# Kernel tuning notes

Measured on AMD Instinct MI355X. Metric: run time of the kernel, lower is better.

## Reference

```python
import jax, jax.numpy as jnp
import numpy as np

D, H, W, C = 24, 24, 16, 2        # image_dims + num_classes
THETA_ALPHA = 160.0               # bilateral spatial std
THETA_BETA = 3.0                  # bilateral intensity std
THETA_GAMMA = 3.0                 # spatial-only std
NUM_ITERATIONS = 5
N = D * H * W


def _gauss_kernel(feats):
    # Dense Gaussian kernel K_ij = exp(-0.5 * ||f_i - f_j||^2).
    # This is the exact filter that the permutohedral lattice approximates
    # (self-term included, matching the lattice splat/blur/slice behaviour).
    sq = jnp.sum(feats * feats, axis=-1)               # [N]
    d2 = sq[:, None] + sq[None, :] - 2.0 * feats @ feats.T
    return jnp.exp(-0.5 * jnp.maximum(d2, 0.0))        # [N, N]


def _positions():
    zz, yy, xx = jnp.meshgrid(jnp.arange(D), jnp.arange(H), jnp.arange(W), indexing='ij')
    return jnp.stack([zz, yy, xx], axis=-1).reshape(N, 3).astype(jnp.float32)


def setup_inputs() -> dict:
    key = jax.random.key(0)
    k1, k2 = jax.random.split(key)
    unaries = jax.random.normal(k1, (1, D, H, W, C), dtype=jnp.float32)
    rgb = jax.random.uniform(k2, (1, D, H, W, 1), dtype=jnp.float32)
    # learned params (build() initial values)
    spatial_ker_weights = jnp.array([1.41, 1.41], dtype=jnp.float32)
    bilateral_ker_weights = jnp.array([3.85, 3.85], dtype=jnp.float32)
    compatibility_matrix = jnp.eye(C, dtype=jnp.float32)
    return dict(unaries=unaries, rgb=rgb,
                spatial_ker_weights=spatial_ker_weights,
                bilateral_ker_weights=bilateral_ker_weights,
                compatibility_matrix=compatibility_matrix)


def reference(unaries, rgb, spatial_ker_weights, bilateral_ker_weights, compatibility_matrix):
    out_shape = unaries.shape
    u = unaries.reshape(N, C)                 # batch index 0 only, as in the TF code
    img = rgb.reshape(N, -1)
    pos = _positions()

    Ks = _gauss_kernel(pos / THETA_GAMMA)                                        # spatial kernel [N,N]
    Kb = _gauss_kernel(jnp.concatenate([pos / THETA_ALPHA, img / THETA_BETA], -1))  # bilateral kernel [N,N]

    # normalization = filter applied to all-ones (row sums)
    norm_s = jnp.sum(Ks, axis=-1, keepdims=True)   # [N,1]
    norm_b = jnp.sum(Kb, axis=-1, keepdims=True)   # [N,1]

    q = u
    for _ in range(NUM_ITERATIONS):
        spatial_out = (Ks @ q) / norm_s            # [N,C]
        bilateral_out = (Kb @ q) / norm_b          # [N,C]
        # diag(w_s) @ spatial.T + diag(w_b) @ bilateral.T  ==  per-class scaling
        message = spatial_out * spatial_ker_weights + bilateral_out * bilateral_ker_weights
        pairwise = message @ compatibility_matrix.T  # (compat @ msg.T).T
        q = u - pairwise
    return q.reshape(out_shape)
```

## Files before the change

### kernel.cpp

```cpp
#include <hip/hip_runtime.h>


#define DD 24
#define HH 24
#define WW 16
#define SLICE 384
#define NPTS 9216
#define NT 5
#define NF_ITER 12
#define LOG2E 1.4426950408889634f
#define K3L   (LOG2E / 18.0f)
#define K160L (LOG2E / 51200.0f)

static __device__ __forceinline__ int iabs(int a) { return a < 0 ? -a : a; }

__global__ __launch_bounds__(SLICE)
void xy_kernel(const float2* __restrict__ qsrc,
               const float* __restrict__ rgb,
               float* __restrict__ tmp, int mode) {
    __shared__ float g[DD];
    __shared__ float a[SLICE];
    __shared__ float b[SLICE];
    const int z = blockIdx.x;
    const int f = blockIdx.y;
    const int t = threadIdx.x;

    const bool spatial = (mode == 1) && (f < 2);
    const float k2 = spatial ? K3L : K160L;
    if (t < DD) g[t] = exp2f(-(float)(t * t) * k2);

    const int i = z * SLICE + t;
    float v;
    if (mode == 0) {
        float I3 = rgb[i] * (1.0f / 3.0f);
        float E = exp2f(-0.5f * LOG2E * I3 * I3);
        float P = E;
        for (int s = 0; s < f; ++s) P *= I3;
        v = P;
    } else {
        float2 q = qsrc[i];
        if (f < 2) {
            v = (f == 0) ? q.x : q.y;
        } else {
            int tt = (f - 2) >> 1;
            int c  = (f - 2) & 1;
            float I3 = rgb[i] * (1.0f / 3.0f);
            float E = exp2f(-0.5f * LOG2E * I3 * I3);
            float P = E;
            for (int s = 0; s < tt; ++s) P *= I3;
            v = P * (c ? q.y : q.x);
        }
    }
    a[t] = v;
    __syncthreads();

    const int y = t >> 4, x = t & 15;
    float s = 0.f;
#pragma unroll
    for (int xp = 0; xp < WW; ++xp)
        s = fmaf(g[iabs(x - xp)], a[(y << 4) + xp], s);
    b[t] = s;
    __syncthreads();

    float s2 = 0.f;
#pragma unroll
    for (int yp = 0; yp < HH; ++yp)
        s2 = fmaf(g[iabs(y - yp)], b[(yp << 4) + x], s2);
    tmp[f * NPTS + i] = s2;
}

__global__ __launch_bounds__(256)
void z_norm_kernel(const float* __restrict__ tmp,
                   const float* __restrict__ rgb,
                   float* __restrict__ norm_b) {
    __shared__ float gz[DD];
    const int tid = threadIdx.x;
    const int i = blockIdx.x * 256 + tid;
    const int z = i / SLICE;
    const int yx = i - z * SLICE;
    if (tid < DD) gz[tid] = exp2f(-(float)(tid * tid) * K160L);
    __syncthreads();

    float acc[NT] = {0.f, 0.f, 0.f, 0.f, 0.f};
    for (int zp = 0; zp < DD; ++zp) {
        float w = gz[iabs(z - zp)];
        const float* base = tmp + zp * SLICE + yx;
#pragma unroll
        for (int t = 0; t < NT; ++t) acc[t] = fmaf(w, base[t * NPTS], acc[t]);
    }
    const float invf[NT] = {1.f, 1.f, 0.5f, 1.f / 6.f, 1.f / 24.f};
    float I3 = rgb[i] * (1.0f / 3.0f);
    float P = exp2f(-0.5f * LOG2E * I3 * I3);
    float nb = 0.f;
#pragma unroll
    for (int t = 0; t < NT; ++t) { nb = fmaf(P * invf[t], acc[t], nb); P *= I3; }
    norm_b[i] = nb;
}

__global__ __launch_bounds__(256)
void z_iter_kernel(const float* __restrict__ tmp,
                   const float* __restrict__ rgb,
                   const float* __restrict__ norm_b,
                   const float2* __restrict__ u2,
                   const float* __restrict__ sw,
                   const float* __restrict__ bw,
                   const float* __restrict__ compat,
                   float2* __restrict__ qdst,
                   float2* __restrict__ out) {
    __shared__ float g3[DD];
    __shared__ float g160[DD];
    __shared__ float ssx[WW];
    __shared__ float ssy[HH];
    const int tid = threadIdx.x;
    const int i = blockIdx.x * 256 + tid;
    const int z = i / SLICE;
    const int yx = i - z * SLICE;
    const int y = yx >> 4, x = yx & 15;

    if (tid < DD) g3[tid] = exp2f(-(float)(tid * tid) * K3L);
    else if (tid >= 32 && tid < 32 + DD) {
        int d = tid - 32;
        g160[d] = exp2f(-(float)(d * d) * K160L);
    }
    __syncthreads();
    if (tid < WW) {
        float s = 0.f;
        for (int xp = 0; xp < WW; ++xp) s += g3[iabs(tid - xp)];
        ssx[tid] = s;
    } else if (tid >= 64 && tid < 64 + HH) {
        int yy = tid - 64;
        float s = 0.f;
        for (int yp = 0; yp < HH; ++yp) s += g3[iabs(yy - yp)];
        ssy[yy] = s;
    }
    __syncthreads();

    float acc[NF_ITER];
#pragma unroll
    for (int f = 0; f < NF_ITER; ++f) acc[f] = 0.f;
    for (int zp = 0; zp < DD; ++zp) {
        float w3 = g3[iabs(z - zp)];
        float wb = g160[iabs(z - zp)];
        const float* base = tmp + zp * SLICE + yx;
        acc[0] = fmaf(w3, base[0 * NPTS], acc[0]);
        acc[1] = fmaf(w3, base[1 * NPTS], acc[1]);
#pragma unroll
        for (int f = 2; f < NF_ITER; ++f) acc[f] = fmaf(wb, base[f * NPTS], acc[f]);
    }

    float inv_ns = 1.0f / (ssy[z] * ssy[y] * ssx[x]);
    float s0 = acc[0] * inv_ns;
    float s1 = acc[1] * inv_ns;

    const float invf[NT] = {1.f, 1.f, 0.5f, 1.f / 6.f, 1.f / 24.f};
    float I3 = rgb[i] * (1.0f / 3.0f);
    float P = exp2f(-0.5f * LOG2E * I3 * I3);
    float b0 = 0.f, b1 = 0.f;
#pragma unroll
    for (int t = 0; t < NT; ++t) {
        float w = P * invf[t];
        b0 = fmaf(w, acc[2 + 2 * t], b0);
        b1 = fmaf(w, acc[3 + 2 * t], b1);
        P *= I3;
    }
    float inv_nb = 1.0f / norm_b[i];
    b0 *= inv_nb;
    b1 *= inv_nb;

    float m0 = s0 * sw[0] + b0 * bw[0];
    float m1 = s1 * sw[1] + b1 * bw[1];
    float p0 = fmaf(compat[0], m0, compat[1] * m1);
    float p1 = fmaf(compat[2], m0, compat[3] * m1);
    float2 uu = u2[i];
    float2 qn = make_float2(uu.x - p0, uu.y - p1);
    qdst[i] = qn;
    if (out != nullptr) out[i] = qn;
}

extern "C" void kernel_launch(void* const* d_in, const int* in_sizes, int n_in,
                              void* d_out, int out_size, void* d_ws, size_t ws_size,
                              hipStream_t stream) {
    const float*  u      = (const float*)d_in[0];
    const float*  rgb    = (const float*)d_in[1];
    const float*  sw     = (const float*)d_in[2];
    const float*  bw     = (const float*)d_in[3];
    const float*  compat = (const float*)d_in[4];
    const float2* u2     = (const float2*)u;
    float2* out = (float2*)d_out;

    float* ws = (float*)d_ws;
    float*  tmp    = ws;
    float*  norm_b = ws + NF_ITER * NPTS;
    float2* qbuf   = (float2*)(ws + (NF_ITER + 1) * NPTS);

    xy_kernel<<<dim3(DD, NT), SLICE, 0, stream>>>(nullptr, rgb, tmp, 0);
    z_norm_kernel<<<NPTS / 256, 256, 0, stream>>>(tmp, rgb, norm_b);

    for (int it = 0; it < 5; ++it) {
        const float2* qsrc = (it == 0) ? u2 : (const float2*)qbuf;
        xy_kernel<<<dim3(DD, NF_ITER), SLICE, 0, stream>>>(qsrc, rgb, tmp, 1);
        z_iter_kernel<<<NPTS / 256, 256, 0, stream>>>(tmp, rgb, norm_b, u2,
                                                      sw, bw, compat, qbuf,
                                                      (it == 4) ? out : nullptr);
    }
}
```

Measured before the change: 118.1 us.

## Fuse all CRF stages into one persistent kernel with grid barriers

Replaces the twelve separate launches (xy, z_norm, and five xy/z_iter pairs) with one persistent 24-block kernel that keeps per-point state in registers and synchronises between stages with an atomic grid barrier. The intermediate layout changes to point-major with 12 interleaved features read and written as float4, and all 12 features are convolved in one block per z-slice rather than one block per feature. The aim is to remove launch and inter-kernel gaps. In exchange only 24 workgroups run, using a small fraction of the GPU, and the kernel relies on all blocks being co-resident for the spin barrier.

```diff
diff --git a/kernel.cpp b/kernel.cpp
--- a/kernel.cpp
+++ b/kernel.cpp
@@ -7,200 +7,259 @@
 #define SLICE 384
 #define NPTS 9216
 #define NT 5
-#define NF_ITER 12
+#define TP 12
+#define NP 8
+#define LPITCH 196
+#define NBLOCKS 24
 #define LOG2E 1.4426950408889634f
 #define K3L   (LOG2E / 18.0f)
 #define K160L (LOG2E / 51200.0f)
 
 static __device__ __forceinline__ int iabs(int a) { return a < 0 ? -a : a; }
 
-__global__ __launch_bounds__(SLICE)
-void xy_kernel(const float2* __restrict__ qsrc,
-               const float* __restrict__ rgb,
-               float* __restrict__ tmp, int mode) {
-    __shared__ float g[DD];
-    __shared__ float a[SLICE];
-    __shared__ float b[SLICE];
+__global__ void init_bar_kernel(unsigned* bar) {
+    if (threadIdx.x < 8) bar[threadIdx.x] = 0u;
+}
+
+static __device__ __forceinline__ void gridbar(unsigned* bar, int phase) {
+    __syncthreads();
+    if (threadIdx.x == 0) {
+        __threadfence();
+        __hip_atomic_fetch_add(&bar[phase], 1u, __ATOMIC_ACQ_REL,
+                               __HIP_MEMORY_SCOPE_AGENT);
+        while (__hip_atomic_load(&bar[phase], __ATOMIC_ACQUIRE,
+                                 __HIP_MEMORY_SCOPE_AGENT) < (unsigned)NBLOCKS) {
+            __builtin_amdgcn_s_sleep(1);
+        }
+        __threadfence();
+    }
+    __syncthreads();
+}
+
+static __device__ __forceinline__ void xy_conv12(
+        float* sA, float* sB, const float* g3, const float* g160,
+        int y, int x, const float v[12], float ov[12]) {
+    float4* wrow = (float4*)(sA + y * LPITCH + x * 12);
+    wrow[0] = make_float4(v[0], v[1], v[2], v[3]);
+    wrow[1] = make_float4(v[4], v[5], v[6], v[7]);
+    wrow[2] = make_float4(v[8], v[9], v[10], v[11]);
+    __syncthreads();
+
+    float ax[12];
+#pragma unroll
+    for (int f = 0; f < 12; ++f) ax[f] = 0.f;
+    const float4* rowy = (const float4*)(sA + y * LPITCH);
+#pragma unroll
+    for (int xp = 0; xp < WW; ++xp) {
+        int d = iabs(x - xp);
+        float w3 = g3[d], wb = g160[d];
+        float4 a0 = rowy[xp * 3 + 0];
+        float4 a1 = rowy[xp * 3 + 1];
+        float4 a2 = rowy[xp * 3 + 2];
+        ax[0] = fmaf(w3, a0.x, ax[0]);  ax[1] = fmaf(w3, a0.y, ax[1]);
+        ax[2] = fmaf(wb, a0.z, ax[2]);  ax[3] = fmaf(wb, a0.w, ax[3]);
+        ax[4] = fmaf(wb, a1.x, ax[4]);  ax[5] = fmaf(wb, a1.y, ax[5]);
+        ax[6] = fmaf(wb, a1.z, ax[6]);  ax[7] = fmaf(wb, a1.w, ax[7]);
+        ax[8] = fmaf(wb, a2.x, ax[8]);  ax[9] = fmaf(wb, a2.y, ax[9]);
+        ax[10] = fmaf(wb, a2.z, ax[10]); ax[11] = fmaf(wb, a2.w, ax[11]);
+    }
+    float4* wrowB = (float4*)(sB + y * LPITCH + x * 12);
+    wrowB[0] = make_float4(ax[0], ax[1], ax[2], ax[3]);
+    wrowB[1] = make_float4(ax[4], ax[5], ax[6], ax[7]);
+    wrowB[2] = make_float4(ax[8], ax[9], ax[10], ax[11]);
+    __syncthreads();
+
+#pragma unroll
+    for (int f = 0; f < 12; ++f) ov[f] = 0.f;
+#pragma unroll
+    for (int yp = 0; yp < HH; ++yp) {
+        int d = iabs(y - yp);
+        float w3 = g3[d], wb = g160[d];
+        const float4* col = (const float4*)(sB + yp * LPITCH + x * 12);
+        float4 b0 = col[0];
+        float4 b1 = col[1];
+        float4 b2 = col[2];
+        ov[0] = fmaf(w3, b0.x, ov[0]);  ov[1] = fmaf(w3, b0.y, ov[1]);
+        ov[2] = fmaf(wb, b0.z, ov[2]);  ov[3] = fmaf(wb, b0.w, ov[3]);
+        ov[4] = fmaf(wb, b1.x, ov[4]);  ov[5] = fmaf(wb, b1.y, ov[5]);
+        ov[6] = fmaf(wb, b1.z, ov[6]);  ov[7] = fmaf(wb, b1.w, ov[7]);
+        ov[8] = fmaf(wb, b2.x, ov[8]);  ov[9] = fmaf(wb, b2.y, ov[9]);
+        ov[10] = fmaf(wb, b2.z, ov[10]); ov[11] = fmaf(wb, b2.w, ov[11]);
+    }
+    __syncthreads();
+}
+
+__global__ __launch_bounds__(384, 1)
+void crf_persist(const float2* __restrict__ u2, const float* __restrict__ rgb,
+                 const float* __restrict__ sw, const float* __restrict__ bw,
+                 const float* __restrict__ compat,
+                 float* __restrict__ tmpA, float* __restrict__ tmpB,
+                 float* __restrict__ tmpN, unsigned* __restrict__ bar,
+                 float2* __restrict__ out) {
+    __shared__ float g3[32];
+    __shared__ float g160[32];
+    __shared__ float sA[HH * LPITCH];
+    __shared__ float sB[HH * LPITCH];
+
     const int z = blockIdx.x;
-    const int f = blockIdx.y;
     const int t = threadIdx.x;
-
-    const bool spatial = (mode == 1) && (f < 2);
-    const float k2 = spatial ? K3L : K160L;
-    if (t < DD) g[t] = exp2f(-(float)(t * t) * k2);
-
+    const int y = t >> 4;
+    const int x = t & 15;
     const int i = z * SLICE + t;
-    float v;
-    if (mode == 0) {
-        float I3 = rgb[i] * (1.0f / 3.0f);
-        float E = exp2f(-0.5f * LOG2E * I3 * I3);
-        float P = E;
-        for (int s = 0; s < f; ++s) P *= I3;
-        v = P;
-    } else {
-        float2 q = qsrc[i];
-        if (f < 2) {
-            v = (f == 0) ? q.x : q.y;
-        } else {
-            int tt = (f - 2) >> 1;
-            int c  = (f - 2) & 1;
-            float I3 = rgb[i] * (1.0f / 3.0f);
-            float E = exp2f(-0.5f * LOG2E * I3 * I3);
-            float P = E;
-            for (int s = 0; s < tt; ++s) P *= I3;
-            v = P * (c ? q.y : q.x);
-        }
-    }
-    a[t] = v;
-    __syncthreads();
-
-    const int y = t >> 4, x = t & 15;
-    float s = 0.f;
-#pragma unroll
-    for (int xp = 0; xp < WW; ++xp)
-        s = fmaf(g[iabs(x - xp)], a[(y << 4) + xp], s);
-    b[t] = s;
-    __syncthreads();
-
-    float s2 = 0.f;
-#pragma unroll
-    for (int yp = 0; yp < HH; ++yp)
-        s2 = fmaf(g[iabs(y - yp)], b[(yp << 4) + x], s2);
-    tmp[f * NPTS + i] = s2;
-}
-
-__global__ __launch_bounds__(256)
-void z_norm_kernel(const float* __restrict__ tmp,
-                   const float* __restrict__ rgb,
-                   float* __restrict__ norm_b) {
-    __shared__ float gz[DD];
-    const int tid = threadIdx.x;
-    const int i = blockIdx.x * 256 + tid;
-    const int z = i / SLICE;
-    const int yx = i - z * SLICE;
-    if (tid < DD) gz[tid] = exp2f(-(float)(tid * tid) * K160L);
-    __syncthreads();
-
-    float acc[NT] = {0.f, 0.f, 0.f, 0.f, 0.f};
-    for (int zp = 0; zp < DD; ++zp) {
-        float w = gz[iabs(z - zp)];
-        const float* base = tmp + zp * SLICE + yx;
-#pragma unroll
-        for (int t = 0; t < NT; ++t) acc[t] = fmaf(w, base[t * NPTS], acc[t]);
-    }
+
+    if (t < DD) {
+        g3[t] = exp2f(-(float)(t * t) * K3L);
+        g160[t] = exp2f(-(float)(t * t) * K160L);
+    }
+    __syncthreads();
+
+    float sx = 0.f, sy = 0.f, sz = 0.f;
+    for (int xp = 0; xp < WW; ++xp) sx += g3[iabs(x - xp)];
+    for (int yp = 0; yp < HH; ++yp) sy += g3[iabs(y - yp)];
+    for (int zp = 0; zp < DD; ++zp) sz += g3[iabs(z - zp)];
+    const float inv_ns = 1.0f / (sx * sy * sz);
+    const float I3 = rgb[i] * (1.0f / 3.0f);
+    const float E = exp2f(-0.5f * LOG2E * I3 * I3);
+    const float2 uu = u2[i];
+    const float sw0 = sw[0], sw1 = sw[1];
+    const float bw0 = bw[0], bw1 = bw[1];
+    const float c00 = compat[0], c01 = compat[1];
+    const float c10 = compat[2], c11 = compat[3];
     const float invf[NT] = {1.f, 1.f, 0.5f, 1.f / 6.f, 1.f / 24.f};
-    float I3 = rgb[i] * (1.0f / 3.0f);
-    float P = exp2f(-0.5f * LOG2E * I3 * I3);
-    float nb = 0.f;
-#pragma unroll
-    for (int t = 0; t < NT; ++t) { nb = fmaf(P * invf[t], acc[t], nb); P *= I3; }
-    norm_b[i] = nb;
-}
-
-__global__ __launch_bounds__(256)
-void z_iter_kernel(const float* __restrict__ tmp,
-                   const float* __restrict__ rgb,
-                   const float* __restrict__ norm_b,
-                   const float2* __restrict__ u2,
-                   const float* __restrict__ sw,
-                   const float* __restrict__ bw,
-                   const float* __restrict__ compat,
-                   float2* __restrict__ qdst,
-                   float2* __restrict__ out) {
-    __shared__ float g3[DD];
-    __shared__ float g160[DD];
-    __shared__ float ssx[WW];
-    __shared__ float ssy[HH];
-    const int tid = threadIdx.x;
-    const int i = blockIdx.x * 256 + tid;
-    const int z = i / SLICE;
-    const int yx = i - z * SLICE;
-    const int y = yx >> 4, x = yx & 15;
-
-    if (tid < DD) g3[tid] = exp2f(-(float)(tid * tid) * K3L);
-    else if (tid >= 32 && tid < 32 + DD) {
-        int d = tid - 32;
-        g160[d] = exp2f(-(float)(d * d) * K160L);
-    }
-    __syncthreads();
-    if (tid < WW) {
-        float s = 0.f;
-        for (int xp = 0; xp < WW; ++xp) s += g3[iabs(tid - xp)];
-        ssx[tid] = s;
-    } else if (tid >= 64 && tid < 64 + HH) {
-        int yy = tid - 64;
-        float s = 0.f;
-        for (int yp = 0; yp < HH; ++yp) s += g3[iabs(yy - yp)];
-        ssy[yy] = s;
-    }
-    __syncthreads();
-
-    float acc[NF_ITER];
-#pragma unroll
-    for (int f = 0; f < NF_ITER; ++f) acc[f] = 0.f;
-    for (int zp = 0; zp < DD; ++zp) {
-        float w3 = g3[iabs(z - zp)];
-        float wb = g160[iabs(z - zp)];
-        const float* base = tmp + zp * SLICE + yx;
-        acc[0] = fmaf(w3, base[0 * NPTS], acc[0]);
-        acc[1] = fmaf(w3, base[1 * NPTS], acc[1]);
-#pragma unroll
-        for (int f = 2; f < NF_ITER; ++f) acc[f] = fmaf(wb, base[f * NPTS], acc[f]);
-    }
-
-    float inv_ns = 1.0f / (ssy[z] * ssy[y] * ssx[x]);
-    float s0 = acc[0] * inv_ns;
-    float s1 = acc[1] * inv_ns;
-
-    const float invf[NT] = {1.f, 1.f, 0.5f, 1.f / 6.f, 1.f / 24.f};
-    float I3 = rgb[i] * (1.0f / 3.0f);
-    float P = exp2f(-0.5f * LOG2E * I3 * I3);
-    float b0 = 0.f, b1 = 0.f;
-#pragma unroll
-    for (int t = 0; t < NT; ++t) {
-        float w = P * invf[t];
-        b0 = fmaf(w, acc[2 + 2 * t], b0);
-        b1 = fmaf(w, acc[3 + 2 * t], b1);
-        P *= I3;
-    }
-    float inv_nb = 1.0f / norm_b[i];
-    b0 *= inv_nb;
-    b1 *= inv_nb;
-
-    float m0 = s0 * sw[0] + b0 * bw[0];
-    float m1 = s1 * sw[1] + b1 * bw[1];
-    float p0 = fmaf(compat[0], m0, compat[1] * m1);
-    float p1 = fmaf(compat[2], m0, compat[3] * m1);
-    float2 uu = u2[i];
-    float2 qn = make_float2(uu.x - p0, uu.y - p1);
-    qdst[i] = qn;
-    if (out != nullptr) out[i] = qn;
+    float Pt[NT];
+    Pt[0] = E;
+#pragma unroll
+    for (int k = 1; k < NT; ++k) Pt[k] = Pt[k - 1] * I3;
+
+    float v[12], ov[12];
+
+#pragma unroll
+    for (int f = 0; f < 12; ++f) v[f] = 0.f;
+#pragma unroll
+    for (int k = 0; k < NT; ++k) v[2 + k] = Pt[k];
+    xy_conv12(sA, sB, g3, g160, y, x, v, ov);
+    {
+        float* pn = tmpN + (size_t)i * NP;
+        *(float4*)pn = make_float4(ov[2], ov[3], ov[4], ov[5]);
+        pn[4] = ov[6];
+    }
+    float q0 = uu.x, q1 = uu.y;
+    v[0] = q0; v[1] = q1;
+#pragma unroll
+    for (int k = 0; k < NT; ++k) { v[2 + 2 * k] = Pt[k] * q0; v[3 + 2 * k] = Pt[k] * q1; }
+    xy_conv12(sA, sB, g3, g160, y, x, v, ov);
+    {
+        float4* pd = (float4*)(tmpA + (size_t)i * TP);
+        pd[0] = make_float4(ov[0], ov[1], ov[2], ov[3]);
+        pd[1] = make_float4(ov[4], ov[5], ov[6], ov[7]);
+        pd[2] = make_float4(ov[8], ov[9], ov[10], ov[11]);
+    }
+    gridbar(bar, 0);
+
+    float inv_nb = 0.f;
+    const float* tsrc = tmpA;
+    float* tdst = tmpB;
+
+    for (int it = 0; it < 5; ++it) {
+        if (it == 0) {
+            float accN[NT] = {0.f, 0.f, 0.f, 0.f, 0.f};
+            const float* pn = tmpN + (size_t)t * NP;
+            for (int zp = 0; zp < DD; ++zp) {
+                float wb = g160[iabs(z - zp)];
+                float4 n0 = *(const float4*)pn;
+                float n4 = pn[4];
+                accN[0] = fmaf(wb, n0.x, accN[0]);
+                accN[1] = fmaf(wb, n0.y, accN[1]);
+                accN[2] = fmaf(wb, n0.z, accN[2]);
+                accN[3] = fmaf(wb, n0.w, accN[3]);
+                accN[4] = fmaf(wb, n4, accN[4]);
+                pn += (size_t)SLICE * NP;
+            }
+            float nb = 0.f;
+#pragma unroll
+            for (int k = 0; k < NT; ++k) nb = fmaf(Pt[k] * invf[k], accN[k], nb);
+            inv_nb = 1.0f / nb;
+        }
+
+        float acc[12];
+#pragma unroll
+        for (int f = 0; f < 12; ++f) acc[f] = 0.f;
+        {
+            const float* p = tsrc + (size_t)t * TP;
+            for (int zp = 0; zp < DD; ++zp) {
+                int d = iabs(z - zp);
+                float w3 = g3[d], wb = g160[d];
+                float4 a0 = ((const float4*)p)[0];
+                float4 a1 = ((const float4*)p)[1];
+                float4 a2 = ((const float4*)p)[2];
+                acc[0] = fmaf(w3, a0.x, acc[0]);  acc[1] = fmaf(w3, a0.y, acc[1]);
+                acc[2] = fmaf(wb, a0.z, acc[2]);  acc[3] = fmaf(wb, a0.w, acc[3]);
+                acc[4] = fmaf(wb, a1.x, acc[4]);  acc[5] = fmaf(wb, a1.y, acc[5]);
+                acc[6] = fmaf(wb, a1.z, acc[6]);  acc[7] = fmaf(wb, a1.w, acc[7]);
+                acc[8] = fmaf(wb, a2.x, acc[8]);  acc[9] = fmaf(wb, a2.y, acc[9]);
+                acc[10] = fmaf(wb, a2.z, acc[10]); acc[11] = fmaf(wb, a2.w, acc[11]);
+                p += (size_t)SLICE * TP;
+            }
+        }
+
+        float s0 = acc[0] * inv_ns;
+        float s1 = acc[1] * inv_ns;
+        float b0 = 0.f, b1 = 0.f;
+#pragma unroll
+        for (int k = 0; k < NT; ++k) {
+            float w = Pt[k] * invf[k];
+            b0 = fmaf(w, acc[2 + 2 * k], b0);
+            b1 = fmaf(w, acc[3 + 2 * k], b1);
+        }
+        b0 *= inv_nb;
+        b1 *= inv_nb;
+        float m0 = s0 * sw0 + b0 * bw0;
+        float m1 = s1 * sw1 + b1 * bw1;
+        float p0 = fmaf(c00, m0, c01 * m1);
+        float p1 = fmaf(c10, m0, c11 * m1);
+        q0 = uu.x - p0;
+        q1 = uu.y - p1;
+
+        if (it == 4) {
+            out[i] = make_float2(q0, q1);
+            break;
+        }
+
+        v[0] = q0; v[1] = q1;
+#pragma unroll
+        for (int k = 0; k < NT; ++k) { v[2 + 2 * k] = Pt[k] * q0; v[3 + 2 * k] = Pt[k] * q1; }
+        xy_conv12(sA, sB, g3, g160, y, x, v, ov);
+        {
+            float4* pd = (float4*)(tdst + (size_t)i * TP);
+            pd[0] = make_float4(ov[0], ov[1], ov[2], ov[3]);
+            pd[1] = make_float4(ov[4], ov[5], ov[6], ov[7]);
+            pd[2] = make_float4(ov[8], ov[9], ov[10], ov[11]);
+        }
+        gridbar(bar, 1 + it);
+
+        const float* ns = tdst;
+        tdst = (float*)tsrc;
+        tsrc = ns;
+    }
 }
 
 extern "C" void kernel_launch(void* const* d_in, const int* in_sizes, int n_in,
                               void* d_out, int out_size, void* d_ws, size_t ws_size,
                               hipStream_t stream) {
-    const float*  u      = (const float*)d_in[0];
+    const float2* u2     = (const float2*)d_in[0];
     const float*  rgb    = (const float*)d_in[1];
     const float*  sw     = (const float*)d_in[2];
     const float*  bw     = (const float*)d_in[3];
     const float*  compat = (const float*)d_in[4];
-    const float2* u2     = (const float2*)u;
     float2* out = (float2*)d_out;
 
     float* ws = (float*)d_ws;
-    float*  tmp    = ws;
-    float*  norm_b = ws + NF_ITER * NPTS;
-    float2* qbuf   = (float2*)(ws + (NF_ITER + 1) * NPTS);
-
-    xy_kernel<<<dim3(DD, NT), SLICE, 0, stream>>>(nullptr, rgb, tmp, 0);
-    z_norm_kernel<<<NPTS / 256, 256, 0, stream>>>(tmp, rgb, norm_b);
-
-    for (int it = 0; it < 5; ++it) {
-        const float2* qsrc = (it == 0) ? u2 : (const float2*)qbuf;
-        xy_kernel<<<dim3(DD, NF_ITER), SLICE, 0, stream>>>(qsrc, rgb, tmp, 1);
-        z_iter_kernel<<<NPTS / 256, 256, 0, stream>>>(tmp, rgb, norm_b, u2,
-                                                      sw, bw, compat, qbuf,
-                                                      (it == 4) ? out : nullptr);
-    }
-}
+    float* tmpA = ws;
+    float* tmpB = ws + NPTS * TP;
+    float* tmpN = ws + 2 * NPTS * TP;
+    unsigned* bar = (unsigned*)(ws + 2 * NPTS * TP + NPTS * NP);
+
+    init_bar_kernel<<<1, 64, 0, stream>>>(bar);
+    crf_persist<<<NBLOCKS, 384, 0, stream>>>(u2, rgb, sw, bw, compat,
+                                             tmpA, tmpB, tmpN, bar, out);
+}
```

After: 155.9 us. 1.32x slower.

## Split z-convolution into its own per-feature kernel and merge norm pass into iteration

Applied to the files above, without the earlier changes.

The z-axis Gaussian convolution is moved out of the pointwise update kernel into a separate kernel launched over a grid of slice by feature, so each thread accumulates a single feature instead of twelve. The normalisation features are folded into the first iteration's xy and z passes, which drops the separate norm kernel. Padded shared arrays are used for the xy pass. The cost is one extra launch per iteration and an extra round trip of the intermediate buffer through global memory, in exchange for more parallelism in the z reduction.

```diff
diff --git a/kernel.cpp b/kernel.cpp
--- a/kernel.cpp
+++ b/kernel.cpp
@@ -7,7 +7,8 @@
 #define SLICE 384
 #define NPTS 9216
 #define NT 5
-#define NF_ITER 12
+#define NFI 12
+#define NFT 17
 #define LOG2E 1.4426950408889634f
 #define K3L   (LOG2E / 18.0f)
 #define K160L (LOG2E / 51200.0f)
@@ -15,192 +16,158 @@
 static __device__ __forceinline__ int iabs(int a) { return a < 0 ? -a : a; }
 
 __global__ __launch_bounds__(SLICE)
-void xy_kernel(const float2* __restrict__ qsrc,
-               const float* __restrict__ rgb,
-               float* __restrict__ tmp, int mode) {
-    __shared__ float g[DD];
-    __shared__ float a[SLICE];
-    __shared__ float b[SLICE];
-    const int z = blockIdx.x;
-    const int f = blockIdx.y;
-    const int t = threadIdx.x;
+void k_xy(const float2* __restrict__ qsrc, const float* __restrict__ rgb,
+          float* __restrict__ tmp) {
+    __shared__ float gk[32];
+    __shared__ float sA[HH][WW + 1];
+    __shared__ float sB[HH][WW + 1];
+    const int z = blockIdx.x, f = blockIdx.y, t = threadIdx.x;
+    const int y = t >> 4, x = t & 15;
+    const int i = z * SLICE + t;
 
-    const bool spatial = (mode == 1) && (f < 2);
-    const float k2 = spatial ? K3L : K160L;
-    if (t < DD) g[t] = exp2f(-(float)(t * t) * k2);
+    const float kk = (f < 2) ? K3L : K160L;
+    if (t < DD) gk[t] = exp2f(-(float)(t * t) * kk);
 
-    const int i = z * SLICE + t;
     float v;
-    if (mode == 0) {
-        float I3 = rgb[i] * (1.0f / 3.0f);
+    if (f < 2) {
+        float2 q = qsrc[i];
+        v = (f == 0) ? q.x : q.y;
+    } else {
+        float I3 = rgb[i] * (1.f / 3.f);
         float E = exp2f(-0.5f * LOG2E * I3 * I3);
+        int k = (f < NFI) ? ((f - 2) >> 1) : (f - NFI);
         float P = E;
-        for (int s = 0; s < f; ++s) P *= I3;
-        v = P;
-    } else {
-        float2 q = qsrc[i];
-        if (f < 2) {
-            v = (f == 0) ? q.x : q.y;
+        for (int s = 0; s < k; ++s) P *= I3;
+        if (f < NFI) {
+            float2 q = qsrc[i];
+            v = P * (((f - 2) & 1) ? q.y : q.x);
         } else {
-            int tt = (f - 2) >> 1;
-            int c  = (f - 2) & 1;
-            float I3 = rgb[i] * (1.0f / 3.0f);
-            float E = exp2f(-0.5f * LOG2E * I3 * I3);
-            float P = E;
-            for (int s = 0; s < tt; ++s) P *= I3;
-            v = P * (c ? q.y : q.x);
+            v = P;
         }
     }
-    a[t] = v;
+    sA[y][x] = v;
     __syncthreads();
 
-    const int y = t >> 4, x = t & 15;
-    float s = 0.f;
+    float a = 0.f;
 #pragma unroll
-    for (int xp = 0; xp < WW; ++xp)
-        s = fmaf(g[iabs(x - xp)], a[(y << 4) + xp], s);
-    b[t] = s;
+    for (int xp = 0; xp < WW; ++xp) a = fmaf(gk[iabs(x - xp)], sA[y][xp], a);
+    sB[y][x] = a;
     __syncthreads();
 
-    float s2 = 0.f;
+    float b = 0.f;
 #pragma unroll
-    for (int yp = 0; yp < HH; ++yp)
-        s2 = fmaf(g[iabs(y - yp)], b[(yp << 4) + x], s2);
-    tmp[f * NPTS + i] = s2;
+    for (int yp = 0; yp < HH; ++yp) b = fmaf(gk[iabs(y - yp)], sB[yp][x], b);
+    tmp[f * NPTS + i] = b;
+}
+
+__global__ __launch_bounds__(SLICE)
+void k_zconv(const float* __restrict__ tmp, float* __restrict__ zout) {
+    __shared__ float gk[32];
+    const int z = blockIdx.x, f = blockIdx.y, t = threadIdx.x;
+    const float kk = (f < 2) ? K3L : K160L;
+    if (t < DD) gk[t] = exp2f(-(float)(t * t) * kk);
+    __syncthreads();
+
+    float acc = 0.f;
+    const float* p = tmp + f * NPTS + t;
+#pragma unroll 4
+    for (int zp = 0; zp < DD; ++zp)
+        acc = fmaf(gk[iabs(z - zp)], p[zp * SLICE], acc);
+    zout[f * NPTS + z * SLICE + t] = acc;
 }
 
 __global__ __launch_bounds__(256)
-void z_norm_kernel(const float* __restrict__ tmp,
-                   const float* __restrict__ rgb,
-                   float* __restrict__ norm_b) {
-    __shared__ float gz[DD];
-    const int tid = threadIdx.x;
-    const int i = blockIdx.x * 256 + tid;
-    const int z = i / SLICE;
-    const int yx = i - z * SLICE;
-    if (tid < DD) gz[tid] = exp2f(-(float)(tid * tid) * K160L);
+void k_update(const float* __restrict__ zout, const float* __restrict__ rgb,
+              const float2* __restrict__ u2,
+              const float* __restrict__ sw, const float* __restrict__ bw,
+              const float* __restrict__ compat,
+              float* __restrict__ normb, float2* __restrict__ qnew,
+              float2* __restrict__ out, int it) {
+    __shared__ float g3s[32];
+    const int t = threadIdx.x;
+    const int i = blockIdx.x * 256 + t;
+    if (t < DD) g3s[t] = exp2f(-(float)(t * t) * K3L);
     __syncthreads();
 
-    float acc[NT] = {0.f, 0.f, 0.f, 0.f, 0.f};
-    for (int zp = 0; zp < DD; ++zp) {
-        float w = gz[iabs(z - zp)];
-        const float* base = tmp + zp * SLICE + yx;
-#pragma unroll
-        for (int t = 0; t < NT; ++t) acc[t] = fmaf(w, base[t * NPTS], acc[t]);
-    }
-    const float invf[NT] = {1.f, 1.f, 0.5f, 1.f / 6.f, 1.f / 24.f};
-    float I3 = rgb[i] * (1.0f / 3.0f);
-    float P = exp2f(-0.5f * LOG2E * I3 * I3);
-    float nb = 0.f;
-#pragma unroll
-    for (int t = 0; t < NT; ++t) { nb = fmaf(P * invf[t], acc[t], nb); P *= I3; }
-    norm_b[i] = nb;
-}
-
-__global__ __launch_bounds__(256)
-void z_iter_kernel(const float* __restrict__ tmp,
-                   const float* __restrict__ rgb,
-                   const float* __restrict__ norm_b,
-                   const float2* __restrict__ u2,
-                   const float* __restrict__ sw,
-                   const float* __restrict__ bw,
-                   const float* __restrict__ compat,
-                   float2* __restrict__ qdst,
-                   float2* __restrict__ out) {
-    __shared__ float g3[DD];
-    __shared__ float g160[DD];
-    __shared__ float ssx[WW];
-    __shared__ float ssy[HH];
-    const int tid = threadIdx.x;
-    const int i = blockIdx.x * 256 + tid;
     const int z = i / SLICE;
     const int yx = i - z * SLICE;
     const int y = yx >> 4, x = yx & 15;
 
-    if (tid < DD) g3[tid] = exp2f(-(float)(tid * tid) * K3L);
-    else if (tid >= 32 && tid < 32 + DD) {
-        int d = tid - 32;
-        g160[d] = exp2f(-(float)(d * d) * K160L);
-    }
-    __syncthreads();
-    if (tid < WW) {
-        float s = 0.f;
-        for (int xp = 0; xp < WW; ++xp) s += g3[iabs(tid - xp)];
-        ssx[tid] = s;
-    } else if (tid >= 64 && tid < 64 + HH) {
-        int yy = tid - 64;
-        float s = 0.f;
-        for (int yp = 0; yp < HH; ++yp) s += g3[iabs(yy - yp)];
-        ssy[yy] = s;
-    }
-    __syncthreads();
+    float sx = 0.f, sy = 0.f, sz = 0.f;
+#pragma unroll
+    for (int xp = 0; xp < WW; ++xp) sx += g3s[iabs(x - xp)];
+#pragma unroll
+    for (int yp = 0; yp < HH; ++yp) sy += g3s[iabs(y - yp)];
+#pragma unroll
+    for (int zp = 0; zp < DD; ++zp) sz += g3s[iabs(z - zp)];
+    const float inv_ns = 1.0f / (sx * sy * sz);
 
-    float acc[NF_ITER];
+    const float I3 = rgb[i] * (1.f / 3.f);
+    const float E = exp2f(-0.5f * LOG2E * I3 * I3);
+    float Pt[NT];
+    Pt[0] = E;
 #pragma unroll
-    for (int f = 0; f < NF_ITER; ++f) acc[f] = 0.f;
-    for (int zp = 0; zp < DD; ++zp) {
-        float w3 = g3[iabs(z - zp)];
-        float wb = g160[iabs(z - zp)];
-        const float* base = tmp + zp * SLICE + yx;
-        acc[0] = fmaf(w3, base[0 * NPTS], acc[0]);
-        acc[1] = fmaf(w3, base[1 * NPTS], acc[1]);
+    for (int k = 1; k < NT; ++k) Pt[k] = Pt[k - 1] * I3;
+    const float invf[NT] = {1.f, 1.f, 0.5f, 1.f / 6.f, 1.f / 24.f};
+
+    float inv_nb;
+    if (it == 0) {
+        float nb = 0.f;
 #pragma unroll
-        for (int f = 2; f < NF_ITER; ++f) acc[f] = fmaf(wb, base[f * NPTS], acc[f]);
+        for (int k = 0; k < NT; ++k)
+            nb = fmaf(Pt[k] * invf[k], zout[(NFI + k) * NPTS + i], nb);
+        normb[i] = nb;
+        inv_nb = 1.0f / nb;
+    } else {
+        inv_nb = 1.0f / normb[i];
     }
 
-    float inv_ns = 1.0f / (ssy[z] * ssy[y] * ssx[x]);
-    float s0 = acc[0] * inv_ns;
-    float s1 = acc[1] * inv_ns;
-
-    const float invf[NT] = {1.f, 1.f, 0.5f, 1.f / 6.f, 1.f / 24.f};
-    float I3 = rgb[i] * (1.0f / 3.0f);
-    float P = exp2f(-0.5f * LOG2E * I3 * I3);
     float b0 = 0.f, b1 = 0.f;
 #pragma unroll
-    for (int t = 0; t < NT; ++t) {
-        float w = P * invf[t];
-        b0 = fmaf(w, acc[2 + 2 * t], b0);
-        b1 = fmaf(w, acc[3 + 2 * t], b1);
-        P *= I3;
+    for (int k = 0; k < NT; ++k) {
+        float w = Pt[k] * invf[k];
+        b0 = fmaf(w, zout[(2 + 2 * k) * NPTS + i], b0);
+        b1 = fmaf(w, zout[(3 + 2 * k) * NPTS + i], b1);
     }
-    float inv_nb = 1.0f / norm_b[i];
     b0 *= inv_nb;
     b1 *= inv_nb;
+
+    float s0 = zout[i] * inv_ns;
+    float s1 = zout[NPTS + i] * inv_ns;
 
     float m0 = s0 * sw[0] + b0 * bw[0];
     float m1 = s1 * sw[1] + b1 * bw[1];
     float p0 = fmaf(compat[0], m0, compat[1] * m1);
     float p1 = fmaf(compat[2], m0, compat[3] * m1);
-    float2 uu = u2[i];
+    const float2 uu = u2[i];
     float2 qn = make_float2(uu.x - p0, uu.y - p1);
-    qdst[i] = qn;
-    if (out != nullptr) out[i] = qn;
+    qnew[i] = qn;
+    if (it == 4) out[i] = qn;
 }
 
 extern "C" void kernel_launch(void* const* d_in, const int* in_sizes, int n_in,
                               void* d_out, int out_size, void* d_ws, size_t ws_size,
                               hipStream_t stream) {
-    const float*  u      = (const float*)d_in[0];
+    const float2* u2     = (const float2*)d_in[0];
     const float*  rgb    = (const float*)d_in[1];
     const float*  sw     = (const float*)d_in[2];
     const float*  bw     = (const float*)d_in[3];
     const float*  compat = (const float*)d_in[4];
-    const float2* u2     = (const float2*)u;
     float2* out = (float2*)d_out;
 
     float* ws = (float*)d_ws;
-    float*  tmp    = ws;
-    float*  norm_b = ws + NF_ITER * NPTS;
-    float2* qbuf   = (float2*)(ws + (NF_ITER + 1) * NPTS);
+    float*  tmp   = ws;
+    float*  zout  = ws + NFT * NPTS;
+    float*  normb = ws + 2 * NFT * NPTS;
+    float2* qnew  = (float2*)(ws + 2 * NFT * NPTS + NPTS);
 
-    xy_kernel<<<dim3(DD, NT), SLICE, 0, stream>>>(nullptr, rgb, tmp, 0);
-    z_norm_kernel<<<NPTS / 256, 256, 0, stream>>>(tmp, rgb, norm_b);
+    k_xy<<<dim3(DD, NFT), SLICE, 0, stream>>>(u2, rgb, tmp);
 
     for (int it = 0; it < 5; ++it) {
-        const float2* qsrc = (it == 0) ? u2 : (const float2*)qbuf;
-        xy_kernel<<<dim3(DD, NF_ITER), SLICE, 0, stream>>>(qsrc, rgb, tmp, 1);
-        z_iter_kernel<<<NPTS / 256, 256, 0, stream>>>(tmp, rgb, norm_b, u2,
-                                                      sw, bw, compat, qbuf,
-                                                      (it == 4) ? out : nullptr);
+        k_zconv<<<dim3(DD, it == 0 ? NFT : NFI), SLICE, 0, stream>>>(tmp, zout);
+        k_update<<<NPTS / 256, 256, 0, stream>>>(zout, rgb, u2, sw, bw, compat,
+                                                 normb, qnew, out, it);
+        if (it < 4)
+            k_xy<<<dim3(DD, NFI), SLICE, 0, stream>>>((const float2*)qnew, rgb, tmp);
     }
 }
```

After: 109.4 us. 7.4% less time.
